# Optimization experiments

Hardware: AMD Instinct MI355X
Metric: run time of the kernel (lower is better)

Reference implementation:

```python
import jax, jax.numpy as jnp
import numpy as np

N = 8_000_000  # number of (parent, child, relation) edges
N_RELS = 64
P = 3  # n_polarities


def sparsemax(z):
    # sparsemax along last axis (Martins & Astudillo 2016)
    d = z.shape[-1]
    zs = jnp.sort(z, axis=-1)[..., ::-1]          # descending
    cs = jnp.cumsum(zs, axis=-1)
    k = jnp.arange(1, d + 1, dtype=z.dtype)
    support = 1.0 + k * zs > cs                   # [.., d] bool
    ksup = jnp.sum(support, axis=-1, keepdims=True)  # int, size of support
    tau = (jnp.take_along_axis(cs, ksup - 1, axis=-1) - 1.0) / ksup.astype(z.dtype)
    return jnp.maximum(z - tau, 0.0)


def setup_inputs() -> dict:
    key = jax.random.key(0)
    k1, k2, k3, k4, k5 = jax.random.split(key, 5)
    prnt_probs = jax.random.uniform(k1, (N, P), dtype=jnp.float32)
    child_probs = jax.random.uniform(k2, (N, P), dtype=jnp.float32)
    rels = jax.random.randint(k3, (N,), 0, N_RELS, dtype=jnp.int32)
    # learned params (torch inits to ones/constants; perturb so grads are non-degenerate)
    M = 1.0 + 0.1 * jax.random.normal(k4, (N_RELS, P, P), dtype=jnp.float32)
    beta = jax.random.uniform(k5, (N_RELS, P), dtype=jnp.float32)
    z_epsilon = jnp.float32(0.01)
    scale_factor = jnp.float32(21.0)
    return {"prnt_probs": prnt_probs, "child_probs": child_probs, "M": M,
            "beta": beta, "z_epsilon": z_epsilon, "scale_factor": scale_factor,
            "rels": rels, "var_sfx": 0}


def reference(prnt_probs, child_probs, M, beta, z_epsilon, scale_factor, rels, var_sfx):
    # All rows of child_probs/prnt_probs are nonzero (uniform fill), so the
    # nonzero() gathers select every edge and the copy branch is empty:
    # this is the dense alpha path of AlphaModel.forward.
    c = jnp.einsum('nij,nj->ni', M[rels], child_probs)  # relation-gated bmm
    c = sparsemax(c)
    c = sparsemax(c)  # alpha branch re-applies sparsemax (idempotent but faithful)
    p = sparsemax(prnt_probs)
    b = beta[rels]
    alpha = (1.0 - b) * p + b * c
    # scale(): entropy of clamped mixture + cosine similarity
    z = jnp.maximum(p + c, jax.lax.stop_gradient(z_epsilon))  # torch uses .item() -> no grad
    z = z / jnp.sum(z, axis=-1, keepdims=True)
    entropy = -jnp.sum(z * jnp.log(z), axis=-1)
    cos = jnp.sum(p * c, axis=-1)
    norm = jnp.maximum(jnp.linalg.norm(p, axis=-1) * jnp.linalg.norm(c, axis=-1), 1e-10)
    cos = 0.1 + cos / norm
    scale = scale_factor * cos / entropy
    alpha = jnp.maximum(alpha * scale[:, None], 0.001)
    return alpha
```

## Files before the change

kernel.cpp:

```cpp
#include <hip/hip_runtime.h>

#define NRELS 64
#define BLOCK 256

__device__ __forceinline__ float fast_ln(float x) {
    return 0.69314718056f * __builtin_amdgcn_logf(x);
}
__device__ __forceinline__ float fast_rcp(float x) {
    return __builtin_amdgcn_rcpf(x);
}
__device__ __forceinline__ float fast_rsq(float x) {
    return __builtin_amdgcn_rsqf(x);
}

__device__ __forceinline__ void sparsemax3(float z0, float z1, float z2,
                                           float& o0, float& o1, float& o2) {
    float lo01 = fminf(z0, z1), hi01 = fmaxf(z0, z1);
    float s2 = fminf(lo01, z2);
    float mx = fmaxf(lo01, z2);
    float s0 = fmaxf(hi01, mx);
    float s1 = fminf(hi01, mx);
    float cs2 = s0 + s1;
    float cs3 = cs2 + s2;
    bool k2 = (1.0f + 2.0f * s1 > cs2);
    bool k3 = (1.0f + 3.0f * s2 > cs3);
    int k = 1 + (int)k2 + (int)k3;
    float csk = (k == 1) ? s0 : ((k == 2) ? cs2 : cs3);
    float rk  = (k == 1) ? 1.0f : ((k == 2) ? 0.5f : 0.33333334f);
    float tau = (csk - 1.0f) * rk;
    o0 = fmaxf(z0 - tau, 0.0f);
    o1 = fmaxf(z1 - tau, 0.0f);
    o2 = fmaxf(z2 - tau, 0.0f);
}

__device__ __forceinline__ void edge_compute(
    float p0, float p1, float p2,
    float q0, float q1, float q2,
    int r, const float* sM, const float* sB,
    float zeps, float sf,
    float& a0o, float& a1o, float& a2o) {
    const float4 ma = *(const float4*)&sM[r * 12];
    const float4 mb = *(const float4*)&sM[r * 12 + 4];
    const float  m22 = sM[r * 12 + 8];
    float c0 = ma.x * q0 + ma.y * q1 + ma.z * q2;
    float c1 = ma.w * q0 + mb.x * q1 + mb.y * q2;
    float c2 = mb.z * q0 + mb.w * q1 + m22 * q2;
    sparsemax3(c0, c1, c2, c0, c1, c2);
    sparsemax3(c0, c1, c2, c0, c1, c2);
    sparsemax3(p0, p1, p2, p0, p1, p2);
    const float4 bv = *(const float4*)&sB[r * 4];
    float a0 = (1.0f - bv.x) * p0 + bv.x * c0;
    float a1 = (1.0f - bv.y) * p1 + bv.y * c1;
    float a2 = (1.0f - bv.z) * p2 + bv.z * c2;
    float z0 = fmaxf(p0 + c0, zeps);
    float z1 = fmaxf(p1 + c1, zeps);
    float z2 = fmaxf(p2 + c2, zeps);
    float rs = fast_rcp(z0 + z1 + z2);
    z0 *= rs; z1 *= rs; z2 *= rs;
    float ent = -(z0 * fast_ln(z0) + z1 * fast_ln(z1) + z2 * fast_ln(z2));
    float dot = p0 * c0 + p1 * c1 + p2 * c2;
    float pp = p0 * p0 + p1 * p1 + p2 * p2;
    float cc = c0 * c0 + c1 * c1 + c2 * c2;
    float cosv = 0.1f + dot * fast_rsq(fmaxf(pp * cc, 1e-20f));
    float scale = sf * cosv * fast_rcp(ent);
    a0o = fmaxf(a0 * scale, 0.001f);
    a1o = fmaxf(a1 * scale, 0.001f);
    a2o = fmaxf(a2 * scale, 0.001f);
}

__global__ __launch_bounds__(BLOCK) void alpha_kernel(
    const float* __restrict__ prnt, const float* __restrict__ child,
    const float* __restrict__ Mg, const float* __restrict__ betag,
    const float* __restrict__ zeps_p, const float* __restrict__ sf_p,
    const int* __restrict__ rels, float* __restrict__ out, int n_edges) {
    __shared__ __align__(16) float sM[NRELS * 12];
    __shared__ __align__(16) float sB[NRELS * 4];
    for (int i = threadIdx.x; i < NRELS * 9; i += BLOCK) {
        int r = i / 9, rem = i - r * 9;
        sM[r * 12 + rem] = Mg[i];
    }
    for (int i = threadIdx.x; i < NRELS * 3; i += BLOCK) {
        int r = i / 3, rem = i - r * 3;
        sB[r * 4 + rem] = betag[i];
    }
    __syncthreads();

    const float zeps = zeps_p[0];
    const float sf   = sf_p[0];
    const int nt4 = n_edges >> 2;
    int t = blockIdx.x * BLOCK + threadIdx.x;

    if (t < nt4) {
        const float4* p4 = (const float4*)prnt;
        const float4* c4 = (const float4*)child;
        float4* o4 = (float4*)out;
        int4 r4 = ((const int4*)rels)[t];
        float4 pa = p4[3 * t + 0], pb = p4[3 * t + 1], pc = p4[3 * t + 2];
        float4 ca = c4[3 * t + 0], cb = c4[3 * t + 1], cc = c4[3 * t + 2];
        float P[12] = {pa.x, pa.y, pa.z, pa.w, pb.x, pb.y, pb.z, pb.w,
                       pc.x, pc.y, pc.z, pc.w};
        float C[12] = {ca.x, ca.y, ca.z, ca.w, cb.x, cb.y, cb.z, cb.w,
                       cc.x, cc.y, cc.z, cc.w};
        int R[4] = {r4.x, r4.y, r4.z, r4.w};
        float O[12];
        #pragma unroll
        for (int e = 0; e < 4; e++) {
            edge_compute(P[3 * e], P[3 * e + 1], P[3 * e + 2],
                         C[3 * e], C[3 * e + 1], C[3 * e + 2],
                         R[e], sM, sB, zeps, sf,
                         O[3 * e], O[3 * e + 1], O[3 * e + 2]);
        }
        float4 oa = {O[0], O[1], O[2],  O[3]};
        float4 ob = {O[4], O[5], O[6],  O[7]};
        float4 oc = {O[8], O[9], O[10], O[11]};
        o4[3 * t + 0] = oa;
        o4[3 * t + 1] = ob;
        o4[3 * t + 2] = oc;
    } else if (t == nt4) {
        for (int e = nt4 * 4; e < n_edges; e++) {
            float a0, a1, a2;
            edge_compute(prnt[3 * e], prnt[3 * e + 1], prnt[3 * e + 2],
                         child[3 * e], child[3 * e + 1], child[3 * e + 2],
                         rels[e], sM, sB, zeps, sf, a0, a1, a2);
            out[3 * e] = a0; out[3 * e + 1] = a1; out[3 * e + 2] = a2;
        }
    }
}

extern "C" void kernel_launch(void* const* d_in, const int* in_sizes, int n_in,
                              void* d_out, int out_size, void* d_ws, size_t ws_size,
                              hipStream_t stream) {
    const float* prnt  = (const float*)d_in[0];
    const float* child = (const float*)d_in[1];
    const float* Mg    = (const float*)d_in[2];
    const float* betag = (const float*)d_in[3];
    const float* zeps  = (const float*)d_in[4];
    const float* sf    = (const float*)d_in[5];
    const int*   rels  = (const int*)d_in[6];
    float* out = (float*)d_out;

    int n_edges = in_sizes[0] / 3;
    int nthreads = (n_edges >> 2) + 1;
    int nblocks = (nthreads + BLOCK - 1) / BLOCK;
    alpha_kernel<<<nblocks, BLOCK, 0, stream>>>(
        prnt, child, Mg, betag, zeps, sf, rels, out, n_edges);
}
```

Measured before the change: 264.0 us.

## Hold relation tables in lane registers and gather with ds_bpermute, drop redundant sparsemax

Each wave lane loads one relation's 3x3 M matrix and beta row into registers. Per-edge parameters are then gathered with ds_bpermute instead of being read from a shared-memory table, which removes the shared-memory fill and the __syncthreads. The second, idempotent sparsemax on c is dropped, and the beta mix is rewritten as p + b*(c-p). Thread indices are clamped so every thread does the loads and compute, and only valid threads store. The cost is 12 bpermutes per edge in place of a few wide LDS reads, and these still go through LDS hardware.

```diff
diff --git a/kernel.cpp b/kernel.cpp
--- a/kernel.cpp
+++ b/kernel.cpp
@@ -1,6 +1,5 @@
 #include <hip/hip_runtime.h>
 
-#define NRELS 64
 #define BLOCK 256
 
 __device__ __forceinline__ float fast_ln(float x) {
@@ -11,6 +10,10 @@
 }
 __device__ __forceinline__ float fast_rsq(float x) {
     return __builtin_amdgcn_rsqf(x);
+}
+
+__device__ __forceinline__ float bperm(int ab, float v) {
+    return __int_as_float(__builtin_amdgcn_ds_bpermute(ab, __float_as_int(v)));
 }
 
 __device__ __forceinline__ void sparsemax3(float z0, float z1, float z2,
@@ -33,25 +36,24 @@
     o2 = fmaxf(z2 - tau, 0.0f);
 }
 
-__device__ __forceinline__ void edge_compute(
+__device__ __forceinline__ void edge_core(
     float p0, float p1, float p2,
     float q0, float q1, float q2,
-    int r, const float* sM, const float* sB,
+    float m00, float m01, float m02,
+    float m10, float m11, float m12,
+    float m20, float m21, float m22,
+    float b0, float b1, float b2,
     float zeps, float sf,
-    float& a0o, float& a1o, float& a2o) {
-    const float4 ma = *(const float4*)&sM[r * 12];
-    const float4 mb = *(const float4*)&sM[r * 12 + 4];
-    const float  m22 = sM[r * 12 + 8];
-    float c0 = ma.x * q0 + ma.y * q1 + ma.z * q2;
-    float c1 = ma.w * q0 + mb.x * q1 + mb.y * q2;
-    float c2 = mb.z * q0 + mb.w * q1 + m22 * q2;
-    sparsemax3(c0, c1, c2, c0, c1, c2);
+    float& a0o, float& a1o, float& a2o)
+{
+    float c0 = m00 * q0 + m01 * q1 + m02 * q2;
+    float c1 = m10 * q0 + m11 * q1 + m12 * q2;
+    float c2 = m20 * q0 + m21 * q1 + m22 * q2;
     sparsemax3(c0, c1, c2, c0, c1, c2);
     sparsemax3(p0, p1, p2, p0, p1, p2);
-    const float4 bv = *(const float4*)&sB[r * 4];
-    float a0 = (1.0f - bv.x) * p0 + bv.x * c0;
-    float a1 = (1.0f - bv.y) * p1 + bv.y * c1;
-    float a2 = (1.0f - bv.z) * p2 + bv.z * c2;
+    float a0 = p0 + b0 * (c0 - p0);
+    float a1 = p1 + b1 * (c1 - p1);
+    float a2 = p2 + b2 * (c2 - p2);
     float z0 = fmaxf(p0 + c0, zeps);
     float z1 = fmaxf(p1 + c1, zeps);
     float z2 = fmaxf(p2 + c2, zeps);
@@ -72,57 +74,71 @@
     const float* __restrict__ prnt, const float* __restrict__ child,
     const float* __restrict__ Mg, const float* __restrict__ betag,
     const float* __restrict__ zeps_p, const float* __restrict__ sf_p,
-    const int* __restrict__ rels, float* __restrict__ out, int n_edges) {
-    __shared__ __align__(16) float sM[NRELS * 12];
-    __shared__ __align__(16) float sB[NRELS * 4];
-    for (int i = threadIdx.x; i < NRELS * 9; i += BLOCK) {
-        int r = i / 9, rem = i - r * 9;
-        sM[r * 12 + rem] = Mg[i];
+    const int* __restrict__ rels, float* __restrict__ out, int n_edges)
+{
+    const int lane = threadIdx.x & 63;
+    float mt[9], bt[3];
+    {
+        const float* mr = Mg + lane * 9;
+#pragma unroll
+        for (int k = 0; k < 9; ++k) mt[k] = mr[k];
+        const float* br = betag + lane * 3;
+#pragma unroll
+        for (int k = 0; k < 3; ++k) bt[k] = br[k];
     }
-    for (int i = threadIdx.x; i < NRELS * 3; i += BLOCK) {
-        int r = i / 3, rem = i - r * 3;
-        sB[r * 4 + rem] = betag[i];
-    }
-    __syncthreads();
 
     const float zeps = zeps_p[0];
     const float sf   = sf_p[0];
     const int nt4 = n_edges >> 2;
-    int t = blockIdx.x * BLOCK + threadIdx.x;
+    const int t = blockIdx.x * BLOCK + threadIdx.x;
 
-    if (t < nt4) {
+    if (nt4 > 0) {
+        const int tc = min(t, nt4 - 1);
         const float4* p4 = (const float4*)prnt;
         const float4* c4 = (const float4*)child;
-        float4* o4 = (float4*)out;
-        int4 r4 = ((const int4*)rels)[t];
-        float4 pa = p4[3 * t + 0], pb = p4[3 * t + 1], pc = p4[3 * t + 2];
-        float4 ca = c4[3 * t + 0], cb = c4[3 * t + 1], cc = c4[3 * t + 2];
+        int4 r4 = ((const int4*)rels)[tc];
+        float4 pa = p4[3 * tc + 0], pb = p4[3 * tc + 1], pc = p4[3 * tc + 2];
+        float4 ca = c4[3 * tc + 0], cb = c4[3 * tc + 1], cc = c4[3 * tc + 2];
         float P[12] = {pa.x, pa.y, pa.z, pa.w, pb.x, pb.y, pb.z, pb.w,
                        pc.x, pc.y, pc.z, pc.w};
         float C[12] = {ca.x, ca.y, ca.z, ca.w, cb.x, cb.y, cb.z, cb.w,
                        cc.x, cc.y, cc.z, cc.w};
         int R[4] = {r4.x, r4.y, r4.z, r4.w};
         float O[12];
-        #pragma unroll
-        for (int e = 0; e < 4; e++) {
-            edge_compute(P[3 * e], P[3 * e + 1], P[3 * e + 2],
-                         C[3 * e], C[3 * e + 1], C[3 * e + 2],
-                         R[e], sM, sB, zeps, sf,
-                         O[3 * e], O[3 * e + 1], O[3 * e + 2]);
+#pragma unroll
+        for (int e = 0; e < 4; ++e) {
+            int ab = R[e] << 2;
+            float g0 = bperm(ab, mt[0]), g1 = bperm(ab, mt[1]), g2 = bperm(ab, mt[2]);
+            float g3 = bperm(ab, mt[3]), g4 = bperm(ab, mt[4]), g5 = bperm(ab, mt[5]);
+            float g6 = bperm(ab, mt[6]), g7 = bperm(ab, mt[7]), g8 = bperm(ab, mt[8]);
+            float h0 = bperm(ab, bt[0]), h1 = bperm(ab, bt[1]), h2 = bperm(ab, bt[2]);
+            edge_core(P[3 * e], P[3 * e + 1], P[3 * e + 2],
+                      C[3 * e], C[3 * e + 1], C[3 * e + 2],
+                      g0, g1, g2, g3, g4, g5, g6, g7, g8,
+                      h0, h1, h2, zeps, sf,
+                      O[3 * e], O[3 * e + 1], O[3 * e + 2]);
         }
-        float4 oa = {O[0], O[1], O[2],  O[3]};
-        float4 ob = {O[4], O[5], O[6],  O[7]};
-        float4 oc = {O[8], O[9], O[10], O[11]};
-        o4[3 * t + 0] = oa;
-        o4[3 * t + 1] = ob;
-        o4[3 * t + 2] = oc;
-    } else if (t == nt4) {
-        for (int e = nt4 * 4; e < n_edges; e++) {
-            float a0, a1, a2;
-            edge_compute(prnt[3 * e], prnt[3 * e + 1], prnt[3 * e + 2],
-                         child[3 * e], child[3 * e + 1], child[3 * e + 2],
-                         rels[e], sM, sB, zeps, sf, a0, a1, a2);
-            out[3 * e] = a0; out[3 * e + 1] = a1; out[3 * e + 2] = a2;
+        if (t < nt4) {
+            float4* o4 = (float4*)out;
+            float4 oa = {O[0], O[1], O[2],  O[3]};
+            float4 ob = {O[4], O[5], O[6],  O[7]};
+            float4 oc = {O[8], O[9], O[10], O[11]};
+            o4[3 * t + 0] = oa;
+            o4[3 * t + 1] = ob;
+            o4[3 * t + 2] = oc;
+        }
+        if (t == nt4) {
+            for (int e = nt4 * 4; e < n_edges; ++e) {
+                int r = rels[e];
+                const float* m = Mg + r * 9;
+                const float* b = betag + r * 3;
+                float a0, a1, a2;
+                edge_core(prnt[3 * e], prnt[3 * e + 1], prnt[3 * e + 2],
+                          child[3 * e], child[3 * e + 1], child[3 * e + 2],
+                          m[0], m[1], m[2], m[3], m[4], m[5], m[6], m[7], m[8],
+                          b[0], b[1], b[2], zeps, sf, a0, a1, a2);
+                out[3 * e] = a0; out[3 * e + 1] = a1; out[3 * e + 2] = a2;
+            }
         }
     }
 }
```

Result: no change. 265.5 us (+0.5%).
